# Kernel tuning notes

Measured on AMD Instinct MI355X. Metric: run time of the kernel, lower is better.

## Reference

```python
import jax, jax.numpy as jnp
import numpy as np

B, N, D = 8, 4096, 256   # batch, nodes, input = hidden = output dim
TD, GD, L = 64, 73, 2    # topo_dim, gdv_dim, num_passes
NEG = -1e9               # fp32 mask value from get_mask_value


def setup_inputs() -> dict:
    key = jax.random.key(0)
    ks = jax.random.split(key, 24)
    s = 0.05
    nrm = lambda k, shp: jax.random.normal(k, shp, jnp.float32) * s
    d = {}
    d['x'] = jax.random.normal(ks[0], (B, N, D), jnp.float32)
    d['adj'] = jax.random.randint(ks[1], (D, D), 0, 2, jnp.int32)
    d['gdv'] = jax.random.uniform(ks[2], (D, GD), dtype=jnp.float32)
    d['W_in'] = nrm(ks[3], (D, D));   d['b_in'] = nrm(ks[4], (D,))
    d['W_out'] = nrm(ks[5], (D, D)); d['b_out'] = nrm(ks[6], (D,))
    d['g1_W'] = nrm(ks[7], (GD, TD));  d['g1_b'] = nrm(ks[8], (TD,))
    d['g2_W'] = nrm(ks[9], (TD, TD));  d['g2_b'] = nrm(ks[10], (TD,))
    d['gres_W'] = nrm(ks[11], (GD, TD)); d['gres_b'] = nrm(ks[12], (TD,))
    d['ln_g'] = jnp.ones((D,), jnp.float32); d['ln_b'] = jnp.zeros((D,), jnp.float32)
    d['Wf'] = nrm(ks[13], (L, D, D)); d['bf'] = nrm(ks[14], (L, D))
    d['Wt'] = nrm(ks[15], (L, TD, D)); d['bt'] = nrm(ks[16], (L, D))
    d['wa_feat'] = nrm(ks[17], (L, 2 * D)); d['ba_feat'] = nrm(ks[18], (L,))
    d['wa_topo'] = nrm(ks[19], (L, 2 * D)); d['ba_topo'] = nrm(ks[20], (L,))
    d['Wo'] = nrm(ks[21], (L, D, D)); d['bo'] = nrm(ks[22], (L, D))
    d['lng'] = jnp.ones((L, D), jnp.float32); d['lnb'] = jnp.zeros((L, D), jnp.float32)
    return d


def _ln(x, g, b, eps=1e-5):
    m = x.mean(-1, keepdims=True)
    v = ((x - m) ** 2).mean(-1, keepdims=True)
    return (x - m) * jax.lax.rsqrt(v + eps) * g + b


def reference(x, adj, gdv, W_in, b_in, W_out, b_out, g1_W, g1_b, g2_W, g2_b,
              gres_W, gres_b, ln_g, ln_b, Wf, bf, Wt, bt, wa_feat, ba_feat,
              wa_topo, ba_topo, Wo, bo, lng, lnb):
    # GDV -> topo embedding; batch-independent, so keep it [D, TD] instead of
    # the original's broadcast [B, D, TD] (same math, no duplicated compute).
    g = gdv / (gdv.sum(1, keepdims=True) + 1e-6)
    t = jax.nn.relu(g @ g1_W + g1_b) @ g2_W + g2_b + (g @ gres_W + gres_b)  # [D, TD]
    mask = adj == 0  # [D, D]
    h = x @ W_in + b_in  # [B, N, D]
    for l in range(L):
        Tp = t @ Wt[l] + bt[l]  # [D, D] topo projection (hidden_dim == D)
        # topo_attn Linear(2D,1) on cat([T_i, T_j]) == (Tp@w_i)_i + (Tp@w_j)_j + bias
        wi, wj = wa_topo[l, :D], wa_topo[l, D:]
        e_topo = jax.nn.leaky_relu((Tp @ wi)[:, None] + (Tp @ wj)[None, :] + ba_topo[l])
        beta = jax.nn.softmax(jnp.where(mask, NEG, e_topo), axis=-1)  # [D, D]
        T_out = beta @ Tp  # [D, D]
        Hp = h @ Wf[l] + bf[l]  # [B, N, D]
        # feature_attn Linear(2D,1) on cat([H_n, T_f]) decomposed the same way
        wh, wt = wa_feat[l, :D], wa_feat[l, D:]
        e_feat = jax.nn.leaky_relu((Hp @ wh)[:, :, None] + (T_out @ wt)[None, None, :] + ba_feat[l])
        alpha = jax.nn.softmax(e_feat, axis=-1)  # [B, N, D]
        h_new = jnp.einsum('bnf,fh->bnh', alpha, T_out)
        # output proj + residual (input==output -> plain add), dropout = identity (eval)
        h = _ln(h_new @ Wo[l] + bo[l] + h, lng[l], lnb[l])
    return _ln(h @ W_out + b_out, ln_g, ln_b)
```

## Files before the change

kernel.cpp:

```cpp
#include <hip/hip_runtime.h>
#include <hip/hip_bf16.h>


typedef float f32x4 __attribute__((ext_vector_type(4)));
typedef short bf16x8 __attribute__((ext_vector_type(8)));

__device__ __forceinline__ unsigned short f2bf(float f) {
  unsigned int u = __builtin_bit_cast(unsigned int, f);
  u += 0x7FFFu + ((u >> 16) & 1u);
  return (unsigned short)(u >> 16);
}
__device__ __forceinline__ float bf2f(unsigned short u) {
  return __builtin_bit_cast(float, (unsigned int)u << 16);
}
__device__ __forceinline__ float lrelu(float x) { return x > 0.f ? x : 0.01f * x; }

template <int CTRL>
__device__ __forceinline__ float dpp_ror_add(float v) {
  int s = __builtin_amdgcn_update_dpp(0, __builtin_bit_cast(int, v), CTRL, 0xf, 0xf, true);
  return v + __builtin_bit_cast(float, s);
}
__device__ __forceinline__ float sum16(float v) {
  v = dpp_ror_add<0x128>(v);
  v = dpp_ror_add<0x124>(v);
  v = dpp_ror_add<0x122>(v);
  v = dpp_ror_add<0x121>(v);
  return v;
}

__device__ __forceinline__ float block_sum(float v, float* s4, int t) {
  v = sum16(v);
  v += __shfl_xor(v, 16, 64);
  v += __shfl_xor(v, 32, 64);
  __syncthreads();
  if ((t & 63) == 0) s4[t >> 6] = v;
  __syncthreads();
  return s4[0] + s4[1] + s4[2] + s4[3];
}
__device__ __forceinline__ float block_max(float v, float* s4, int t) {
#pragma unroll
  for (int m = 1; m < 64; m <<= 1) v = fmaxf(v, __shfl_xor(v, m, 64));
  __syncthreads();
  if ((t & 63) == 0) s4[t >> 6] = v;
  __syncthreads();
  return fmaxf(fmaxf(s4[0], s4[1]), fmaxf(s4[2], s4[3]));
}

__device__ __forceinline__ int swz_off(int k, int n) {
  return ((((k >> 5) * 16 + (n >> 4)) * 4 + ((k >> 3) & 3)) * 16 + (n & 15)) * 8 + (k & 7);
}
__device__ __forceinline__ int alds_byte(int n, int m) {
  int grp = n >> 3;
  int base = (grp * 32 + m) * 16 + (n & 7) * 2;
  return base ^ ((grp & 7) << 4);
}

__global__ void ta_kernel(const float* __restrict__ gdv,
                          const float* __restrict__ g1W, const float* __restrict__ g1b,
                          const float* __restrict__ g2W, const float* __restrict__ g2b,
                          const float* __restrict__ grW, const float* __restrict__ grb,
                          const float* __restrict__ Wt, const float* __restrict__ bt,
                          const float* __restrict__ wat,
                          float* __restrict__ Tp, float* __restrict__ pb, float* __restrict__ qb) {
  int l = blockIdx.x >> 8, i = blockIdx.x & 255, t = threadIdx.x;
  __shared__ float gs[73], as_[64], ts[64], s4[4];
  float gv = (t < 73) ? gdv[i * 73 + t] : 0.f;
  float gsum = block_sum(gv, s4, t);
  if (t < 73) gs[t] = gv / (gsum + 1e-6f);
  __syncthreads();
  if (t < 64) {
    float a = g1b[t], gr = grb[t];
    for (int k = 0; k < 73; ++k) { float gk = gs[k]; a = fmaf(gk, g1W[k * 64 + t], a); gr = fmaf(gk, grW[k * 64 + t], gr); }
    as_[t] = fmaxf(a, 0.f);
    ts[t] = gr + g2b[t];
  }
  __syncthreads();
  float tv = 0.f;
  if (t < 64) {
    tv = ts[t];
    for (int k = 0; k < 64; ++k) tv = fmaf(as_[k], g2W[k * 64 + t], tv);
  }
  __syncthreads();
  if (t < 64) ts[t] = tv;
  __syncthreads();
  float tp = bt[l * 256 + t];
  for (int k = 0; k < 64; ++k) tp = fmaf(ts[k], Wt[(l * 64 + k) * 256 + t], tp);
  Tp[(l * 256 + i) * 256 + t] = tp;
  float pp = block_sum(tp * wat[l * 512 + t], s4, t);
  float qq = block_sum(tp * wat[l * 512 + 256 + t], s4, t);
  if (t == 0) { pb[l * 256 + i] = pp; qb[l * 256 + i] = qq; }
}

__global__ void tb_kernel(const int* __restrict__ adj, const float* __restrict__ Tp,
                          const float* __restrict__ pb, const float* __restrict__ qb,
                          const float* __restrict__ batopo, const float* __restrict__ Wo,
                          const float* __restrict__ wafeat, const float* __restrict__ bafeat,
                          const float* __restrict__ Wf, const float* __restrict__ bfv,
                          const float* __restrict__ Win, const float* __restrict__ Wout,
                          float* __restrict__ rp, float* __restrict__ ub, float* __restrict__ cb,
                          unsigned short* __restrict__ Uws) {
  int b = blockIdx.x, t = threadIdx.x;
  if (b >= 512) {
    int bb = b - 512;
    const float* src = (bb < 16) ? Win : Wout;
    unsigned short* dst = Uws + ((bb < 16) ? 0 : 65536);
    int r0 = (bb & 15) * 16;
    for (int kk = 0; kk < 16; ++kk) {
      int k = r0 + kk;
      dst[swz_off(k, t)] = f2bf(src[k * 256 + t]);
    }
    return;
  }
  int l = b >> 8, i = b & 255;
  __shared__ float beta[256], tout[256], s4[4];
  float e = pb[l * 256 + i] + qb[l * 256 + t] + batopo[l];
  e = lrelu(e);
  if (adj[i * 256 + t] == 0) e = -1e9f;
  float mx = block_max(e, s4, t);
  float w = __expf(e - mx);
  float Z = block_sum(w, s4, t);
  beta[t] = w / Z;
  __syncthreads();
  float acc = 0.f;
  for (int j = 0; j < 256; ++j) acc = fmaf(beta[j], Tp[(l * 256 + j) * 256 + t], acc);
  tout[t] = acc;
  __syncthreads();
  const float* WoL = Wo + l * 65536;
  float macc = 0.f;
  for (int h2 = 0; h2 < 256; ++h2) macc = fmaf(tout[h2], WoL[h2 * 256 + t], macc);
  Uws[131072 + l * 65536 + swz_off(i, t)] = f2bf(macc);
  const float* wf = wafeat + l * 512;
  float rsum = block_sum(tout[t] * wf[256 + t], s4, t);
  if (t == 0) rp[l * 256 + i] = rsum + bafeat[l];
  float usum = block_sum(Wf[(l * 256 + i) * 256 + t] * wf[t], s4, t);
  if (t == 0) ub[l * 256 + i] = usum;
  if (i == 0) {
    float csum = block_sum(bfv[l * 256 + t] * wf[t], s4, t);
    if (t == 0) cb[l] = csum;
  }
}

#define MFMA(A, B, C) __builtin_amdgcn_mfma_f32_16x16x32_bf16(A, B, C, 0, 0, 0)

__device__ __forceinline__ void kloop(const char* smc, const unsigned short* Bws,
                                      int wid, int lane, int li, int g, f32x4 acc[2][2]) {
  const bf16x8* Bw = (const bf16x8*)Bws + wid * 2 * 64 + lane;
  bf16x8 b0a = Bw[0], b1a = Bw[64];
  bf16x8 b0b = Bw[1024], b1b = Bw[1024 + 64];
#pragma unroll
  for (int kb = 0; kb < 8; ++kb) {
    bf16x8 nb0, nb1;
    if (kb < 6) {
      nb0 = Bw[(kb + 2) * 1024];
      nb1 = Bw[(kb + 2) * 1024 + 64];
    }
    int grp = kb * 4 + g;
    int ab = ((grp * 32 + li) * 16) ^ ((grp & 7) << 4);
    bf16x8 a0 = *(const bf16x8*)(smc + ab);
    bf16x8 a1 = *(const bf16x8*)(smc + ab + 256);
    __builtin_amdgcn_s_setprio(1);
    acc[0][0] = MFMA(a0, b0a, acc[0][0]);
    acc[1][0] = MFMA(a1, b0a, acc[1][0]);
    acc[0][1] = MFMA(a0, b1a, acc[0][1]);
    acc[1][1] = MFMA(a1, b1a, acc[1][1]);
    __builtin_amdgcn_s_setprio(0);
    b0a = b0b; b1a = b1b;
    if (kb < 6) { b0b = nb0; b1b = nb1; }
  }
}

#define S_REDUCE(UBARR, CBV)                                                   \
  {                                                                            \
    float u0_ = UBARR[ncol[0]], u1_ = UBARR[ncol[1]];                          \
    _Pragma("unroll") for (int rt = 0; rt < 2; ++rt) {                         \
      float sp[4];                                                             \
      _Pragma("unroll") for (int r = 0; r < 4; ++r)                            \
        sp[r] = h[rt][0][r] * u0_ + h[rt][1][r] * u1_;                         \
      _Pragma("unroll") for (int r = 0; r < 4; ++r) sp[r] = sum16(sp[r]);      \
      if (li == 0) {                                                           \
        _Pragma("unroll") for (int r = 0; r < 4; ++r)                          \
          red[wid][rt * 16 + g * 4 + r] = sp[r];                               \
      }                                                                        \
    }                                                                          \
    __syncthreads();                                                           \
    if (t < 32) {                                                              \
      float S = 0.f;                                                           \
      _Pragma("unroll") for (int w = 0; w < 8; ++w) S += red[w][t];            \
      row_s[t] = S + (CBV);                                                    \
    }                                                                          \
    __syncthreads();                                                           \
  }

#define LN_STATS()                                                             \
  {                                                                            \
    _Pragma("unroll") for (int rt = 0; rt < 2; ++rt) {                         \
      float sA[4], sQ[4];                                                      \
      _Pragma("unroll") for (int r = 0; r < 4; ++r) {                          \
        float a0 = h[rt][0][r], a1 = h[rt][1][r];                              \
        sA[r] = a0 + a1;                                                       \
        sQ[r] = a0 * a0 + a1 * a1;                                             \
      }                                                                        \
      _Pragma("unroll") for (int r = 0; r < 4; ++r) {                          \
        sA[r] = sum16(sA[r]); sQ[r] = sum16(sQ[r]);                            \
      }                                                                        \
      if (li == 0) {                                                           \
        _Pragma("unroll") for (int r = 0; r < 4; ++r) {                        \
          int row_ = rt * 16 + g * 4 + r;                                      \
          red[wid][row_] = sA[r]; red[8 + wid][row_] = sQ[r];                  \
        }                                                                      \
      }                                                                        \
    }                                                                          \
    __syncthreads();                                                           \
    if (t < 32) {                                                              \
      float S = 0.f, Q = 0.f;                                                  \
      _Pragma("unroll") for (int w = 0; w < 8; ++w) { S += red[w][t]; Q += red[8 + w][t]; } \
      float mean_ = S * (1.f / 256.f);                                         \
      float var_ = Q * (1.f / 256.f) - mean_ * mean_;                          \
      mr_s[t][0] = mean_; mr_s[t][1] = rsqrtf(var_ + 1e-5f);                   \
    }                                                                          \
    __syncthreads();                                                           \
  }

__global__ __launch_bounds__(512) void fused_kernel(
    const float* __restrict__ x,
    const float* __restrict__ rp, const float* __restrict__ ub, const float* __restrict__ cbp,
    const unsigned short* __restrict__ Uws,
    const float* __restrict__ bin, const float* __restrict__ bo,
    const float* __restrict__ lng, const float* __restrict__ lnb,
    const float* __restrict__ bout, const float* __restrict__ lngf, const float* __restrict__ lnbf,
    float* __restrict__ out) {
  __shared__ unsigned short alds[8192];
  __shared__ float c_bin[256], c_bout[256], c_lngf[256], c_lnbf[256];
  __shared__ float c_ub[2][256], c_bo[2][256], c_lng[2][256], c_lnb[2][256], c_rp[2][256];
  __shared__ float red[16][32];
  __shared__ float row_s[32], invz_s[32];
  __shared__ float mr_s[32][2];
  __shared__ float scal_s[4];
  char* smc = (char*)alds;

  const int wg = blockIdx.x, t = threadIdx.x;
  const int wid = t >> 6, lane = t & 63, li = lane & 15, g = lane >> 4;
  const int rowbase = wg * 32;
  int ncol[2]; ncol[0] = wid * 32 + li; ncol[1] = wid * 32 + 16 + li;

  {
    int ph = wg & 3;
    if (ph > 0) __builtin_amdgcn_s_sleep(24);
    if (ph > 1) __builtin_amdgcn_s_sleep(24);
    if (ph > 2) __builtin_amdgcn_s_sleep(24);
  }

  if (t < 256) {
    c_bin[t] = bin[t]; c_ub[0][t] = ub[t]; c_bo[0][t] = bo[t];
    c_lng[0][t] = lng[t]; c_lnb[0][t] = lnb[t]; c_rp[0][t] = rp[t];
  } else {
    int u = t - 256;
    c_bout[u] = bout[u]; c_lngf[u] = lngf[u]; c_lnbf[u] = lnbf[u];
    c_ub[1][u] = ub[256 + u]; c_bo[1][u] = bo[256 + u];
    c_lng[1][u] = lng[256 + u]; c_lnb[1][u] = lnb[256 + u]; c_rp[1][u] = rp[256 + u];
  }
  if (t == 0) { scal_s[2] = cbp[0]; scal_s[3] = cbp[1]; }

#pragma unroll
  for (int it = 0; it < 4; ++it) {
    int flat = it * 2048 + t * 4;
    int m = flat >> 8, col = flat & 255;
    const f32x4 xv = __builtin_nontemporal_load((const f32x4*)(x + (rowbase + m) * 256 + col));
    ushort4 pk; pk.x = f2bf(xv.x); pk.y = f2bf(xv.y); pk.z = f2bf(xv.z); pk.w = f2bf(xv.w);
    *(ushort4*)(smc + alds_byte(col, m)) = pk;
  }
  __syncthreads();
  if (wid < 2) {
    float m2 = fmaxf(fmaxf(c_rp[wid][lane], c_rp[wid][lane + 64]),
                     fmaxf(c_rp[wid][lane + 128], c_rp[wid][lane + 192]));
#pragma unroll
    for (int mm = 1; mm < 64; mm <<= 1) m2 = fmaxf(m2, __shfl_xor(m2, mm, 64));
    if (lane == 0) scal_s[wid] = m2;
  }

  float h[2][2][4];

  {
    f32x4 acc[2][2];
#pragma unroll
    for (int a = 0; a < 2; ++a)
#pragma unroll
      for (int c = 0; c < 2; ++c) { f32x4 z = {0.f, 0.f, 0.f, 0.f}; acc[a][c] = z; }
    kloop(smc, Uws, wid, lane, li, g, acc);
#pragma unroll
    for (int rt = 0; rt < 2; ++rt)
#pragma unroll
      for (int ct = 0; ct < 2; ++ct)
#pragma unroll
        for (int r = 0; r < 4; ++r) h[rt][ct][r] = acc[rt][ct][r] + c_bin[ncol[ct]];
    S_REDUCE(c_ub[0], scal_s[2]);
  }

#pragma unroll 1
  for (int l = 0; l < 2; ++l) {
    {
      int row = t & 31, p = t >> 5;
      float sm = row_s[row];
      float mx = lrelu(sm + scal_s[l]);
      float z = 0.f;
#pragma unroll
      for (int j = 0; j < 2; ++j) {
        int grp = p * 2 + j;
        float w0 = __expf(lrelu(sm + c_rp[l][grp * 8 + 0]) - mx);
        float w1 = __expf(lrelu(sm + c_rp[l][grp * 8 + 1]) - mx);
        float w2 = __expf(lrelu(sm + c_rp[l][grp * 8 + 2]) - mx);
        float w3 = __expf(lrelu(sm + c_rp[l][grp * 8 + 3]) - mx);
        float w4 = __expf(lrelu(sm + c_rp[l][grp * 8 + 4]) - mx);
        float w5 = __expf(lrelu(sm + c_rp[l][grp * 8 + 5]) - mx);
        float w6 = __expf(lrelu(sm + c_rp[l][grp * 8 + 6]) - mx);
        float w7 = __expf(lrelu(sm + c_rp[l][grp * 8 + 7]) - mx);
        unsigned short u0 = f2bf(w0), u1 = f2bf(w1), u2 = f2bf(w2), u3 = f2bf(w3);
        unsigned short u4 = f2bf(w4), u5 = f2bf(w5), u6 = f2bf(w6), u7 = f2bf(w7);
        z += bf2f(u0) + bf2f(u1) + bf2f(u2) + bf2f(u3) +
             bf2f(u4) + bf2f(u5) + bf2f(u6) + bf2f(u7);
        uint4 pk;
        pk.x = (unsigned int)u0 | ((unsigned int)u1 << 16);
        pk.y = (unsigned int)u2 | ((unsigned int)u3 << 16);
        pk.z = (unsigned int)u4 | ((unsigned int)u5 << 16);
        pk.w = (unsigned int)u6 | ((unsigned int)u7 << 16);
        int byte = ((grp * 32 + row) * 16) ^ ((grp & 7) << 4);
        *(uint4*)(smc + byte) = pk;
      }
      red[p][row] = z;
    }
    __syncthreads();
    if (t < 32) {
      float Z = 0.f;
#pragma unroll
      for (int p = 0; p < 16; ++p) Z += red[p][t];
      invz_s[t] = 1.f / Z;
    }
    __syncthreads();

    f32x4 acc[2][2];
#pragma unroll
    for (int a = 0; a < 2; ++a)
#pragma unroll
      for (int c = 0; c < 2; ++c) { f32x4 z = {0.f, 0.f, 0.f, 0.f}; acc[a][c] = z; }
    kloop(smc, Uws + 131072 + l * 65536, wid, lane, li, g, acc);

#pragma unroll
    for (int rt = 0; rt < 2; ++rt)
#pragma unroll
      for (int r = 0; r < 4; ++r) {
        int row = rt * 16 + g * 4 + r;
        float iz = invz_s[row];
#pragma unroll
        for (int ct = 0; ct < 2; ++ct)
          h[rt][ct][r] = fmaf(acc[rt][ct][r], iz, c_bo[l][ncol[ct]] + h[rt][ct][r]);
      }
    LN_STATS();
#pragma unroll
    for (int rt = 0; rt < 2; ++rt)
#pragma unroll
      for (int r = 0; r < 4; ++r) {
        int row = rt * 16 + g * 4 + r;
        float mean = mr_s[row][0], rstd = mr_s[row][1];
#pragma unroll
        for (int ct = 0; ct < 2; ++ct)
          h[rt][ct][r] = (h[rt][ct][r] - mean) * rstd * c_lng[l][ncol[ct]] + c_lnb[l][ncol[ct]];
      }
    if (l == 0) S_REDUCE(c_ub[1], scal_s[3]);
  }

#pragma unroll
  for (int rt = 0; rt < 2; ++rt)
#pragma unroll
    for (int ct = 0; ct < 2; ++ct)
#pragma unroll
      for (int r = 0; r < 4; ++r) {
        int row = rt * 16 + g * 4 + r;
        *(unsigned short*)(smc + alds_byte(ncol[ct], row)) = f2bf(h[rt][ct][r]);
      }
  __syncthreads();
  {
    f32x4 acc[2][2];
#pragma unroll
    for (int a = 0; a < 2; ++a)
#pragma unroll
      for (int c = 0; c < 2; ++c) { f32x4 z = {0.f, 0.f, 0.f, 0.f}; acc[a][c] = z; }
    kloop(smc, Uws + 65536, wid, lane, li, g, acc);
#pragma unroll
    for (int rt = 0; rt < 2; ++rt)
#pragma unroll
      for (int ct = 0; ct < 2; ++ct)
#pragma unroll
        for (int r = 0; r < 4; ++r) h[rt][ct][r] = acc[rt][ct][r] + c_bout[ncol[ct]];
    LN_STATS();
#pragma unroll
    for (int rt = 0; rt < 2; ++rt)
#pragma unroll
      for (int r = 0; r < 4; ++r) {
        int row = rt * 16 + g * 4 + r;
        float mean = mr_s[row][0], rstd = mr_s[row][1];
#pragma unroll
        for (int ct = 0; ct < 2; ++ct) {
          float v = (h[rt][ct][r] - mean) * rstd * c_lngf[ncol[ct]] + c_lnbf[ncol[ct]];
          __builtin_nontemporal_store(v, out + (rowbase + row) * 256 + ncol[ct]);
        }
      }
  }
}

extern "C" void kernel_launch(void* const* d_in, const int* in_sizes, int n_in,
                              void* d_out, int out_size, void* d_ws, size_t ws_size,
                              hipStream_t stream) {
  const float* x    = (const float*)d_in[0];
  const int*   adj  = (const int*)d_in[1];
  const float* gdv  = (const float*)d_in[2];
  const float* Win  = (const float*)d_in[3];
  const float* bin  = (const float*)d_in[4];
  const float* Wout = (const float*)d_in[5];
  const float* bout = (const float*)d_in[6];
  const float* g1W  = (const float*)d_in[7];
  const float* g1b  = (const float*)d_in[8];
  const float* g2W  = (const float*)d_in[9];
  const float* g2b  = (const float*)d_in[10];
  const float* grW  = (const float*)d_in[11];
  const float* grb  = (const float*)d_in[12];
  const float* lngf = (const float*)d_in[13];
  const float* lnbf = (const float*)d_in[14];
  const float* Wf   = (const float*)d_in[15];
  const float* bfv  = (const float*)d_in[16];
  const float* Wt   = (const float*)d_in[17];
  const float* bt   = (const float*)d_in[18];
  const float* waf  = (const float*)d_in[19];
  const float* baf  = (const float*)d_in[20];
  const float* wat  = (const float*)d_in[21];
  const float* bat  = (const float*)d_in[22];
  const float* Wo   = (const float*)d_in[23];
  const float* bo   = (const float*)d_in[24];
  const float* lng  = (const float*)d_in[25];
  const float* lnb  = (const float*)d_in[26];
  float* out = (float*)d_out;

  float* W = (float*)d_ws;
  float* Tp = W;
  float* pb = W + 131072;
  float* qb = W + 131584;
  float* rp = W + 132096;
  float* ub = W + 132608;
  float* cb = W + 133120;
  unsigned short* Uws = (unsigned short*)(W + 133184);

  ta_kernel<<<512, 256, 0, stream>>>(gdv, g1W, g1b, g2W, g2b, grW, grb, Wt, bt, wat, Tp, pb, qb);
  tb_kernel<<<544, 256, 0, stream>>>(adj, Tp, pb, qb, bat, Wo, waf, baf, Wf, bfv, Win, Wout, rp, ub, cb, Uws);
  fused_kernel<<<1024, 512, 0, stream>>>(x, rp, ub, cb, Uws, bin, bo, lng, lnb, bout, lngf, lnbf, out);
}
```

Measured before the change: 69.57 us.

## Fold next-layer score reduction into LayerNorm stats and use packed bf16 converts

The separate S_REDUCE after layer 0's LayerNorm is removed. The next layer's row score is now computed algebraically from an extra per-row dot product against lng*ub, gathered in the same reduction pass as the LN statistics, which saves a block-wide reduction and its barriers. Manual bf16 rounding is replaced by the hardware v_cvt_pk_bf16_f32 instruction, and the rp values are read with vectorized LDS loads. The staggered-start sleep pattern is also retuned: it now groups blocks by wg>>8 and sleeps longer. The algebraic fold uses the post-normalization identity and can change rounding slightly.

```diff
diff --git a/kernel.cpp b/kernel.cpp
--- a/kernel.cpp
+++ b/kernel.cpp
@@ -5,13 +5,21 @@
 typedef float f32x4 __attribute__((ext_vector_type(4)));
 typedef short bf16x8 __attribute__((ext_vector_type(8)));
 
+__device__ __forceinline__ unsigned int cvt_pk(float lo, float hi) {
+  unsigned int r;
+  asm("v_cvt_pk_bf16_f32 %0, %1, %2" : "=v"(r) : "v"(lo), "v"(hi));
+  return r;
+}
+__device__ __forceinline__ float bfl(unsigned int p) {
+  return __builtin_bit_cast(float, p << 16);
+}
+__device__ __forceinline__ float bfh(unsigned int p) {
+  return __builtin_bit_cast(float, p & 0xFFFF0000u);
+}
 __device__ __forceinline__ unsigned short f2bf(float f) {
   unsigned int u = __builtin_bit_cast(unsigned int, f);
   u += 0x7FFFu + ((u >> 16) & 1u);
   return (unsigned short)(u >> 16);
-}
-__device__ __forceinline__ float bf2f(unsigned short u) {
-  return __builtin_bit_cast(float, (unsigned int)u << 16);
 }
 __device__ __forceinline__ float lrelu(float x) { return x > 0.f ? x : 0.01f * x; }
 
@@ -221,6 +229,43 @@
     __syncthreads();                                                           \
   }
 
+#define LN_STATS3()                                                            \
+  {                                                                            \
+    float gu0 = c_gu[ncol[0]], gu1 = c_gu[ncol[1]];                            \
+    _Pragma("unroll") for (int rt = 0; rt < 2; ++rt) {                         \
+      float sA[4], sQ[4], sG[4];                                               \
+      _Pragma("unroll") for (int r = 0; r < 4; ++r) {                          \
+        float a0 = h[rt][0][r], a1 = h[rt][1][r];                              \
+        sA[r] = a0 + a1;                                                       \
+        sQ[r] = a0 * a0 + a1 * a1;                                             \
+        sG[r] = a0 * gu0 + a1 * gu1;                                           \
+      }                                                                        \
+      _Pragma("unroll") for (int r = 0; r < 4; ++r) {                          \
+        sA[r] = sum16(sA[r]); sQ[r] = sum16(sQ[r]); sG[r] = sum16(sG[r]);      \
+      }                                                                        \
+      if (li == 0) {                                                           \
+        _Pragma("unroll") for (int r = 0; r < 4; ++r) {                        \
+          int row_ = rt * 16 + g * 4 + r;                                      \
+          red[wid][row_] = sA[r]; red[8 + wid][row_] = sQ[r];                  \
+          red[16 + wid][row_] = sG[r];                                         \
+        }                                                                      \
+      }                                                                        \
+    }                                                                          \
+    __syncthreads();                                                           \
+    if (t < 32) {                                                              \
+      float S = 0.f, Q = 0.f, G = 0.f;                                         \
+      _Pragma("unroll") for (int w = 0; w < 8; ++w) {                          \
+        S += red[w][t]; Q += red[8 + w][t]; G += red[16 + w][t];               \
+      }                                                                        \
+      float mean_ = S * (1.f / 256.f);                                         \
+      float var_ = Q * (1.f / 256.f) - mean_ * mean_;                          \
+      float rstd_ = rsqrtf(var_ + 1e-5f);                                      \
+      mr_s[t][0] = mean_; mr_s[t][1] = rstd_;                                  \
+      row_s[t] = rstd_ * (G - mean_ * scal_s[4]) + scal_s[5];                  \
+    }                                                                          \
+    __syncthreads();                                                           \
+  }
+
 __global__ __launch_bounds__(512) void fused_kernel(
     const float* __restrict__ x,
     const float* __restrict__ rp, const float* __restrict__ ub, const float* __restrict__ cbp,
@@ -232,10 +277,11 @@
   __shared__ unsigned short alds[8192];
   __shared__ float c_bin[256], c_bout[256], c_lngf[256], c_lnbf[256];
   __shared__ float c_ub[2][256], c_bo[2][256], c_lng[2][256], c_lnb[2][256], c_rp[2][256];
-  __shared__ float red[16][32];
+  __shared__ float c_gu[256];
+  __shared__ float red[24][32];
   __shared__ float row_s[32], invz_s[32];
   __shared__ float mr_s[32][2];
-  __shared__ float scal_s[4];
+  __shared__ float scal_s[8];
   char* smc = (char*)alds;
 
   const int wg = blockIdx.x, t = threadIdx.x;
@@ -244,10 +290,10 @@
   int ncol[2]; ncol[0] = wid * 32 + li; ncol[1] = wid * 32 + 16 + li;
 
   {
-    int ph = wg & 3;
-    if (ph > 0) __builtin_amdgcn_s_sleep(24);
-    if (ph > 1) __builtin_amdgcn_s_sleep(24);
-    if (ph > 2) __builtin_amdgcn_s_sleep(24);
+    int ph = (wg >> 8) & 3;
+    if (ph > 0) __builtin_amdgcn_s_sleep(39);
+    if (ph > 1) __builtin_amdgcn_s_sleep(39);
+    if (ph > 2) __builtin_amdgcn_s_sleep(39);
   }
 
   if (t < 256) {
@@ -266,8 +312,8 @@
     int flat = it * 2048 + t * 4;
     int m = flat >> 8, col = flat & 255;
     const f32x4 xv = __builtin_nontemporal_load((const f32x4*)(x + (rowbase + m) * 256 + col));
-    ushort4 pk; pk.x = f2bf(xv.x); pk.y = f2bf(xv.y); pk.z = f2bf(xv.z); pk.w = f2bf(xv.w);
-    *(ushort4*)(smc + alds_byte(col, m)) = pk;
+    uint2 pk; pk.x = cvt_pk(xv.x, xv.y); pk.y = cvt_pk(xv.z, xv.w);
+    *(uint2*)(smc + alds_byte(col, m)) = pk;
   }
   __syncthreads();
   if (wid < 2) {
@@ -276,6 +322,20 @@
 #pragma unroll
     for (int mm = 1; mm < 64; mm <<= 1) m2 = fmaxf(m2, __shfl_xor(m2, mm, 64));
     if (lane == 0) scal_s[wid] = m2;
+  } else if (wid == 2) {
+    float ga = 0.f, ba = 0.f;
+#pragma unroll
+    for (int j = 0; j < 4; ++j) {
+      int idx = lane * 4 + j;
+      float u1v = c_ub[1][idx];
+      float gv = c_lng[0][idx] * u1v;
+      c_gu[idx] = gv;
+      ga += gv;
+      ba = fmaf(c_lnb[0][idx], u1v, ba);
+    }
+    ga = sum16(ga); ga += __shfl_xor(ga, 16, 64); ga += __shfl_xor(ga, 32, 64);
+    ba = sum16(ba); ba += __shfl_xor(ba, 16, 64); ba += __shfl_xor(ba, 32, 64);
+    if (lane == 0) { scal_s[4] = ga; scal_s[5] = ba + scal_s[3]; }
   }
 
   float h[2][2][4];
@@ -306,23 +366,21 @@
 #pragma unroll
       for (int j = 0; j < 2; ++j) {
         int grp = p * 2 + j;
-        float w0 = __expf(lrelu(sm + c_rp[l][grp * 8 + 0]) - mx);
-        float w1 = __expf(lrelu(sm + c_rp[l][grp * 8 + 1]) - mx);
-        float w2 = __expf(lrelu(sm + c_rp[l][grp * 8 + 2]) - mx);
-        float w3 = __expf(lrelu(sm + c_rp[l][grp * 8 + 3]) - mx);
-        float w4 = __expf(lrelu(sm + c_rp[l][grp * 8 + 4]) - mx);
-        float w5 = __expf(lrelu(sm + c_rp[l][grp * 8 + 5]) - mx);
-        float w6 = __expf(lrelu(sm + c_rp[l][grp * 8 + 6]) - mx);
-        float w7 = __expf(lrelu(sm + c_rp[l][grp * 8 + 7]) - mx);
-        unsigned short u0 = f2bf(w0), u1 = f2bf(w1), u2 = f2bf(w2), u3 = f2bf(w3);
-        unsigned short u4 = f2bf(w4), u5 = f2bf(w5), u6 = f2bf(w6), u7 = f2bf(w7);
-        z += bf2f(u0) + bf2f(u1) + bf2f(u2) + bf2f(u3) +
-             bf2f(u4) + bf2f(u5) + bf2f(u6) + bf2f(u7);
+        f32x4 ra = *(const f32x4*)&c_rp[l][grp * 8];
+        f32x4 rb = *(const f32x4*)&c_rp[l][grp * 8 + 4];
+        float w0 = __expf(lrelu(sm + ra.x) - mx);
+        float w1 = __expf(lrelu(sm + ra.y) - mx);
+        float w2 = __expf(lrelu(sm + ra.z) - mx);
+        float w3 = __expf(lrelu(sm + ra.w) - mx);
+        float w4 = __expf(lrelu(sm + rb.x) - mx);
+        float w5 = __expf(lrelu(sm + rb.y) - mx);
+        float w6 = __expf(lrelu(sm + rb.z) - mx);
+        float w7 = __expf(lrelu(sm + rb.w) - mx);
         uint4 pk;
-        pk.x = (unsigned int)u0 | ((unsigned int)u1 << 16);
-        pk.y = (unsigned int)u2 | ((unsigned int)u3 << 16);
-        pk.z = (unsigned int)u4 | ((unsigned int)u5 << 16);
-        pk.w = (unsigned int)u6 | ((unsigned int)u7 << 16);
+        pk.x = cvt_pk(w0, w1); pk.y = cvt_pk(w2, w3);
+        pk.z = cvt_pk(w4, w5); pk.w = cvt_pk(w6, w7);
+        z += bfl(pk.x) + bfh(pk.x) + bfl(pk.y) + bfh(pk.y) +
+             bfl(pk.z) + bfh(pk.z) + bfl(pk.w) + bfh(pk.w);
         int byte = ((grp * 32 + row) * 16) ^ ((grp & 7) << 4);
         *(uint4*)(smc + byte) = pk;
       }
@@ -354,7 +412,7 @@
         for (int ct = 0; ct < 2; ++ct)
           h[rt][ct][r] = fmaf(acc[rt][ct][r], iz, c_bo[l][ncol[ct]] + h[rt][ct][r]);
       }
-    LN_STATS();
+    if (l == 0) { LN_STATS3(); } else { LN_STATS(); }
 #pragma unroll
     for (int rt = 0; rt < 2; ++rt)
 #pragma unroll
@@ -365,18 +423,17 @@
         for (int ct = 0; ct < 2; ++ct)
           h[rt][ct][r] = (h[rt][ct][r] - mean) * rstd * c_lng[l][ncol[ct]] + c_lnb[l][ncol[ct]];
       }
-    if (l == 0) S_REDUCE(c_ub[1], scal_s[3]);
   }
 
 #pragma unroll
   for (int rt = 0; rt < 2; ++rt)
 #pragma unroll
-    for (int ct = 0; ct < 2; ++ct)
-#pragma unroll
-      for (int r = 0; r < 4; ++r) {
-        int row = rt * 16 + g * 4 + r;
-        *(unsigned short*)(smc + alds_byte(ncol[ct], row)) = f2bf(h[rt][ct][r]);
-      }
+    for (int r = 0; r < 4; ++r) {
+      int row = rt * 16 + g * 4 + r;
+      unsigned int p = cvt_pk(h[rt][0][r], h[rt][1][r]);
+      *(unsigned short*)(smc + alds_byte(ncol[0], row)) = (unsigned short)p;
+      *(unsigned short*)(smc + alds_byte(ncol[1], row)) = (unsigned short)(p >> 16);
+    }
   __syncthreads();
   {
     f32x4 acc[2][2];
```

Result: faster. 68.02 us (-2.2%).
